# Kernel optimization log

Measured on AMD Instinct MI355X. Metric: run time of the kernel, lower is better.

The kernel has to match this reference:

```python
import jax, jax.numpy as jnp
import numpy as np

N = 8192
NFEAT = 512
NHID = 512
NCLASS = 8
EPS = 1e-9
ADJ_P = 0.01  # edge density


def setup_inputs() -> dict:
    key = jax.random.key(0)
    ks = jax.random.split(key, 16)
    adj = (jax.random.uniform(ks[0], (N, N)) < ADJ_P).astype(jnp.float32)
    x = jax.random.normal(ks[1], (N, NFEAT), dtype=jnp.float32)
    s_in = 1.0 / np.sqrt(NFEAT)
    s_h = 1.0 / np.sqrt(NHID)
    return {
        "adj": adj,
        "x": x,
        "gcn1_W": jax.random.normal(ks[2], (NFEAT, NHID), jnp.float32) * s_in,
        "gcn1_b": jnp.zeros((NHID,), jnp.float32),
        "Qw": jax.random.normal(ks[3], (NHID, NHID), jnp.float32) * s_h,
        "Qb": jnp.zeros((NHID,), jnp.float32),
        "Kw": jax.random.normal(ks[4], (NHID, NHID), jnp.float32) * s_h,
        "Kb": jnp.zeros((NHID,), jnp.float32),
        "Vw": jax.random.normal(ks[5], (NHID, NHID), jnp.float32) * s_h,
        "Vb": jnp.zeros((NHID,), jnp.float32),
        "ln_g": jnp.ones((NHID,), jnp.float32),
        "ln_b": jnp.zeros((NHID,), jnp.float32),
        "gcn2_W": jax.random.normal(ks[6], (NHID, NCLASS), jnp.float32) * s_h,
        "gcn2_b": jnp.zeros((NCLASS,), jnp.float32),
    }


def _gcn_norm(a):
    # symmetric degree normalization D^{-1/2} A D^{-1/2}, degrees = row sums
    d_inv_sqrt = jax.lax.rsqrt(a.sum(axis=1) + EPS)  # [N]
    return d_inv_sqrt[:, None] * a * d_inv_sqrt[None, :]


def _layer_norm(x, g, b):
    mu = x.mean(axis=-1, keepdims=True)
    var = x.var(axis=-1, keepdims=True)
    return (x - mu) * jax.lax.rsqrt(var + 1e-5) * g + b


def reference(adj, x, gcn1_W, gcn1_b, Qw, Qb, Kw, Kb, Vw, Vb, ln_g, ln_b, gcn2_W, gcn2_b):
    # GraphConvolution: adj @ (x W) + b, then ReLU
    h = jax.nn.relu(adj @ (x @ gcn1_W) + gcn1_b)  # [N, NHID]
    Qh = h @ Qw + Qb
    Kh = h @ Kw + Kb
    Vh = h @ Vw + Vb
    # adjacency-masked dense scores (multiplicative mask, as in original)
    A_tilde = adj * (Qh @ Kh.T)  # [N, N]
    attention = jax.nn.softmax(A_tilde, axis=1)
    X_tilde = _gcn_norm(attention) @ Vh  # [N, NHID]
    X_tilde = _layer_norm(X_tilde, ln_g, ln_b)
    z = adj @ (X_tilde @ gcn2_W) + gcn2_b  # [N, NCLASS]
    return jax.nn.softmax(z, axis=1)
```

## Files before the change

kernel.cpp:

```cpp
#include <hip/hip_runtime.h>
#include <math.h>

#define N_NODES 8192
#define NFEAT 512
#define NHID 512
#define NCLASS 8
#define RCAP 192
#define KB_SPLIT 1536
#define KA_SPLIT 1024

__device__ inline ushort f2bf(float f) {
  uint32_t u = __float_as_uint(f);
  uint32_t r = u + 0x7fffu + ((u >> 16) & 1u);
  return (ushort)(r >> 16);
}
__device__ inline float bf2f(ushort h) { return __uint_as_float(((uint32_t)h) << 16); }

__global__ __launch_bounds__(256) void build_ell(const float* __restrict__ adj,
                                                 int* __restrict__ colidx,
                                                 int* __restrict__ deg) {
  int row = blockIdx.x;
  __shared__ int cnt;
  __shared__ int cols[RCAP];
  if (threadIdx.x == 0) cnt = 0;
  __syncthreads();
  const float4* arow = (const float4*)(adj + (size_t)row * N_NODES);
  for (int i = threadIdx.x; i < N_NODES / 4; i += 256) {
    float4 v = arow[i];
    int base = i * 4;
    if (v.x > 0.5f) { int p = atomicAdd(&cnt, 1); if (p < RCAP) cols[p] = base; }
    if (v.y > 0.5f) { int p = atomicAdd(&cnt, 1); if (p < RCAP) cols[p] = base + 1; }
    if (v.z > 0.5f) { int p = atomicAdd(&cnt, 1); if (p < RCAP) cols[p] = base + 2; }
    if (v.w > 0.5f) { int p = atomicAdd(&cnt, 1); if (p < RCAP) cols[p] = base + 3; }
  }
  __syncthreads();
  int d = cnt < RCAP ? cnt : RCAP;
  if (threadIdx.x == 0) deg[row] = d;
  for (int i = threadIdx.x; i < d; i += 256) colidx[(size_t)row * RCAP + i] = cols[i];
}

__global__ void transpose512(const float* __restrict__ in, float* __restrict__ out) {
  __shared__ float tile[32][33];
  int x = blockIdx.x * 32 + threadIdx.x;
  int y0 = blockIdx.y * 32;
  for (int i = threadIdx.y; i < 32; i += 8)
    tile[i][threadIdx.x] = in[(size_t)(y0 + i) * 512 + x];
  __syncthreads();
  int xo = blockIdx.y * 32 + threadIdx.x;
  int yo0 = blockIdx.x * 32;
  for (int i = threadIdx.y; i < 32; i += 8)
    out[(size_t)(yo0 + i) * 512 + xo] = tile[threadIdx.x][i];
}

__global__ __launch_bounds__(256) void sgemm64x128(const float* __restrict__ A,
                                                   const float* __restrict__ B,
                                                   float* __restrict__ C,
                                                   int M, int Nn, int K, int ldc) {
  __shared__ float As[16][68];
  __shared__ float Bs[16][132];
  const int tid = threadIdx.x;
  const int bm = blockIdx.y * 64, bn = blockIdx.x * 128;
  const int tx = tid & 15, ty = tid >> 4;
  const int arow = tid >> 2, acol = (tid & 3) << 2;
  const int brow = tid >> 4, bcol = (tid & 15) << 2;
  float acc[4][8];
#pragma unroll
  for (int i = 0; i < 4; ++i)
#pragma unroll
    for (int j = 0; j < 8; ++j) acc[i][j] = 0.f;
  const float* Ap = A + (size_t)(bm + arow) * K + acol;
  const float* Bp = B + (size_t)brow * Nn + bn + bcol;
  float4 av = *(const float4*)(Ap);
  float4 bv0 = *(const float4*)(Bp);
  float4 bv1 = *(const float4*)(Bp + 64);
  for (int k0 = 0; k0 < K; k0 += 16) {
    if (k0) __syncthreads();
    As[acol + 0][arow] = av.x;
    As[acol + 1][arow] = av.y;
    As[acol + 2][arow] = av.z;
    As[acol + 3][arow] = av.w;
    *(float4*)&Bs[brow][bcol] = bv0;
    *(float4*)&Bs[brow][bcol + 64] = bv1;
    __syncthreads();
    int kn = (k0 + 16 < K) ? k0 + 16 : 0;
    av = *(const float4*)(Ap + kn);
    bv0 = *(const float4*)(Bp + (size_t)kn * Nn);
    bv1 = *(const float4*)(Bp + (size_t)kn * Nn + 64);
#pragma unroll
    for (int kk = 0; kk < 16; ++kk) {
      float4 a = *(const float4*)&As[kk][ty << 2];
      float4 b0 = *(const float4*)&Bs[kk][tx << 2];
      float4 b1 = *(const float4*)&Bs[kk][(tx << 2) + 64];
// ... 96 lines not shown
    for (int j = 0; j < 4; ++j) acc[i][j] = (frag_cd){0.f, 0.f, 0.f, 0.f};

  const int srow = (w << 3) + (lane >> 3);
  const int scolb = (lane & 7) << 4;
  const uint8_t* gA = (const uint8_t*)A + (size_t)(m0 + srow) * (KA_SPLIT * 2) + scolb;
  const uint8_t* gB = (const uint8_t*)Bt + (size_t)(n0 + srow) * (KB_SPLIT * 2) + scolb;

  for (int c = 0; c < 24; ++c) {
    const size_t kaB = (size_t)((c < 8 ? c : c - 8) * 128);
    const size_t kbB = (size_t)(c * 128);
#pragma unroll
    for (int r = 0; r < 4; ++r) {
      __builtin_amdgcn_global_load_lds(
          (const __attribute__((address_space(1))) uint32_t*)(gA + (size_t)(r * 32) * (KA_SPLIT * 2) + kaB),
          (__attribute__((address_space(3))) uint32_t*)((uint8_t*)Atile + r * 4096 + w * 1024), 16, 0, 0);
      __builtin_amdgcn_global_load_lds(
          (const __attribute__((address_space(1))) uint32_t*)(gB + (size_t)(r * 32) * (KB_SPLIT * 2) + kbB),
          (__attribute__((address_space(3))) uint32_t*)((uint8_t*)Btile + r * 4096 + w * 1024), 16, 0, 0);
    }
    __syncthreads();
#pragma unroll
    for (int kk = 0; kk < 2; ++kk) {
      frag_ab af[4], bf[4];
#pragma unroll
      for (int i = 0; i < 4; ++i) {
        af[i] = *(const frag_ab*)((const uint8_t*)Atile + (wm + i * 16 + c16) * 128 + kk * 64 + q * 16);
        bf[i] = *(const frag_ab*)((const uint8_t*)Btile + (wn + i * 16 + c16) * 128 + kk * 64 + q * 16);
      }
#pragma unroll
      for (int i = 0; i < 4; ++i)
#pragma unroll
        for (int j = 0; j < 4; ++j)
          acc[i][j] = __builtin_amdgcn_mfma_f32_16x16x32_bf16(af[i], bf[j], acc[i][j], 0, 0, 0);
    }
    __syncthreads();
  }
#pragma unroll
  for (int j = 0; j < 4; ++j) {
    int col = n0 + wn + j * 16 + c16;
    float bv = bias ? bias[col] : 0.f;
    float csum = 0.f;
#pragma unroll
    for (int i = 0; i < 4; ++i) {
      int row = m0 + wm + i * 16 + q * 4;
#pragma unroll
      for (int r = 0; r < 4; ++r) {
        float v = acc[i][j][r] + bv;
        C[(size_t)(row + r) * ldc + col] = v;
        csum += v;
      }
    }
    if (Tsum && col >= 512) {
      csum += __shfl_xor(csum, 16, 64);
      csum += __shfl_xor(csum, 32, 64);
      if (q == 0) atomicAdd(&Tsum[col - 512], csum);
    }
  }
}

__global__ __launch_bounds__(64) void bias_prep(const float* __restrict__ Qw, const float* __restrict__ Kw,
                                                const float* __restrict__ Qb, const float* __restrict__ Kb,
                                                float* __restrict__ u, float* __restrict__ w,
                                                float* __restrict__ cbuf) {
  int k = blockIdx.x;
  int lane = threadIdx.x;
  if (k == NHID) {
    float s = 0.f;
    for (int j = lane; j < NHID; j += 64) s = fmaf(Qb[j], Kb[j], s);
#pragma unroll
    for (int o = 32; o > 0; o >>= 1) s += __shfl_down(s, o, 64);
    if (lane == 0) cbuf[0] = s;
    return;
  }
  float su = 0.f, sw = 0.f;
  for (int j = lane; j < NHID; j += 64) {
    su = fmaf(Qw[(size_t)k * NHID + j], Kb[j], su);
    sw = fmaf(Kw[(size_t)k * NHID + j], Qb[j], sw);
  }
#pragma unroll
  for (int o = 32; o > 0; o >>= 1) { su += __shfl_down(su, o, 64); sw += __shfl_down(sw, o, 64); }
  if (lane == 0) { u[k] = su; w[k] = sw; }
}

__global__ __launch_bounds__(128) void spmm_fused(const float* __restrict__ xW,
                                                  const int* __restrict__ colidx,
                                                  const int* __restrict__ deg,
                                                  const float* __restrict__ b1,
                                                  const float* __restrict__ u, const float* __restrict__ w,
                                                  float* __restrict__ h, ushort* __restrict__ Hs,
                                                  float* __restrict__ a_vec, float* __restrict__ b_vec) {
  __shared__ int bls[512];
  __shared__ int bcnt[8];
  __shared__ float ra[2], rb[2];
  int row = blockIdx.x, t = threadIdx.x;
  int d = deg[row];
  if (t < 8) bcnt[t] = 0;
  __syncthreads();
  for (int i = t; i < d; i += 128) {
    int c = colidx[(size_t)row * RCAP + i];
    int s = c >> 10;
    int p = atomicAdd(&bcnt[s], 1);
    bls[(s << 6) | p] = c;
  }
  __syncthreads();
  float4 acc = make_float4(0.f, 0.f, 0.f, 0.f);
  int xcd = blockIdx.x & 7;
  for (int k = 0; k < 8; ++k) {
    int s = (xcd + k) & 7;
    int n = bcnt[s];
    const int* bp = &bls[s << 6];
    int e = 0;
    for (; e + 4 <= n; e += 4) {
      float4 v0 = ((const float4*)(xW + (size_t)bp[e + 0] * NHID))[t];
      float4 v1 = ((const float4*)(xW + (size_t)bp[e + 1] * NHID))[t];
      float4 v2 = ((const float4*)(xW + (size_t)bp[e + 2] * NHID))[t];
      float4 v3 = ((const float4*)(xW + (size_t)bp[e + 3] * NHID))[t];
      acc.x += (v0.x + v1.x) + (v2.x + v3.x);
      acc.y += (v0.y + v1.y) + (v2.y + v3.y);
      acc.z += (v0.z + v1.z) + (v2.z + v3.z);
      acc.w += (v0.w + v1.w) + (v2.w + v3.w);
    }
    for (; e < n; ++e) {
      float4 v = ((const float4*)(xW + (size_t)bp[e] * NHID))[t];
      acc.x += v.x; acc.y += v.y; acc.z += v.z; acc.w += v.w;
    }
  }
  float4 bv = ((const float4*)b1)[t];
  float4 o = make_float4(fmaxf(acc.x + bv.x, 0.f), fmaxf(acc.y + bv.y, 0.f),
                         fmaxf(acc.z + bv.z, 0.f), fmaxf(acc.w + bv.w, 0.f));
  ((float4*)(h + (size_t)row * NHID))[t] = o;
  ushort4 hi, lo;
  hi.x = f2bf(o.x); hi.y = f2bf(o.y); hi.z = f2bf(o.z); hi.w = f2bf(o.w);
  lo.x = f2bf(o.x - bf2f(hi.x)); lo.y = f2bf(o.y - bf2f(hi.y));
  lo.z = f2bf(o.z - bf2f(hi.z)); lo.w = f2bf(o.w - bf2f(hi.w));
  ushort* hr = Hs + (size_t)row * KA_SPLIT;
  ((ushort4*)hr)[t] = hi;
  ((ushort4*)(hr + 512))[t] = lo;
  float4 uv = ((const float4*)u)[t], wv4 = ((const float4*)w)[t];
  float sa = fmaf(o.x, uv.x, fmaf(o.y, uv.y, fmaf(o.z, uv.z, o.w * uv.w)));
  float sb = fmaf(o.x, wv4.x, fmaf(o.y, wv4.y, fmaf(o.z, wv4.z, o.w * wv4.w)));
  int wv = t >> 6, lane = t & 63;
#pragma unroll
  for (int off = 32; off > 0; off >>= 1) { sa += __shfl_down(sa, off, 64); sb += __shfl_down(sb, off, 64); }
  if (lane == 0) { ra[wv] = sa; rb[wv] = sb; }
  __syncthreads();
  if (t == 0) { a_vec[row] = ra[0] + ra[1]; b_vec[row] = rb[0] + rb[1]; }
}

__global__ void zero_vec(float* __restrict__ T) { T[threadIdx.x] = 0.f; }

__global__ __launch_bounds__(256) void score_softmax_agg_ln(
    const float* __restrict__ G, int ldg, const float* __restrict__ h,
    const int* __restrict__ colidx, const int* __restrict__ deg,
    const float* __restrict__ a_vec, const float* __restrict__ b_vec,
    const float* __restrict__ cbuf, const float* __restrict__ Vh, int ldv,
    const float* __restrict__ T, const float* __restrict__ lng,
    const float* __restrict__ lnb, float* __restrict__ Xt) {
  __shared__ float gs[4][NHID];
  __shared__ int bls[4][512];
  __shared__ int bcnt[4][8];
  __shared__ int scols[4][RCAP];
  __shared__ float sv[4][RCAP];
  int t = threadIdx.x, wv = t >> 6, lane = t & 63;
  int row = blockIdx.x * 4 + wv;
  int d = deg[row];
  if (lane < 8) bcnt[wv][lane] = 0;
  const float4* gr = (const float4*)(G + (size_t)row * ldg);
  ((float4*)gs[wv])[lane] = gr[lane];
  ((float4*)gs[wv])[64 + lane] = gr[64 + lane];
  __syncthreads();
  for (int i = lane; i < d; i += 64) {
    int c = colidx[(size_t)row * RCAP + i];
    scols[wv][i] = c;
    int s = c >> 10;
    int p = atomicAdd(&bcnt[wv][s], 1);
    bls[wv][(s << 6) | p] = (c << 8) | i;
  }
  __syncthreads();
  float ai = a_vec[row] + cbuf[0];
  int xcd = blockIdx.x & 7;
  int q = lane >> 4, u = lane & 15;
  const float4* gq = (const float4*)gs[wv] + u;
  for (int k = 0; k < 8; ++k) {
    int s = (xcd + k) & 7;
    int n = bcnt[wv][s];
    for (int e0 = 0; e0 < n; e0 += 4) {
      int idx = e0 + q;
      bool act = idx < n;
      int pack = bls[wv][(s << 6) | (act ? idx : 0)];
      int col = pack >> 8;
      const float4* hr = (const float4*)(h + (size_t)col * NHID) + u;
      float s_a = 0.f, s_b = 0.f;
#pragma unroll
      for (int it = 0; it < 8; it += 2) {
        float4 h0 = hr[it * 16], g0 = gq[it * 16];
        float4 h1 = hr[(it + 1) * 16], g1 = gq[(it + 1) * 16];
        s_a = fmaf(h0.x, g0.x, s_a); s_a = fmaf(h0.y, g0.y, s_a);
        s_a = fmaf(h0.z, g0.z, s_a); s_a = fmaf(h0.w, g0.w, s_a);
        s_b = fmaf(h1.x, g1.x, s_b); s_b = fmaf(h1.y, g1.y, s_b);
        s_b = fmaf(h1.z, g1.z, s_b); s_b = fmaf(h1.w, g1.w, s_b);
      }
      float sc = s_a + s_b;
      sc += __shfl_down(sc, 8, 16);
      sc += __shfl_down(sc, 4, 16);
      sc += __shfl_down(sc, 2, 16);
      sc += __shfl_down(sc, 1, 16);
      if (u == 0 && act) sv[wv][pack & 255] = sc + ai + b_vec[col];
    }
  }
  __syncthreads();
  float m = 0.f;
  for (int i = lane; i < d; i += 64) m = fmaxf(m, sv[wv][i]);
#pragma unroll
  for (int o = 32; o > 0; o >>= 1) m = fmaxf(m, __shfl_xor(m, o, 64));
  float ssum = 0.f;
  for (int i = lane; i < d; i += 64) {
    float ex = expf(sv[wv][i] - m);
    sv[wv][i] = ex;
    ssum += ex;
  }
#pragma unroll
  for (int o = 32; o > 0; o >>= 1) ssum += __shfl_xor(ssum, o, 64);
  float em = expf(-m);
  float inv = 1.f / (ssum + (float)(N_NODES - d) * em);
  float ci = em * inv;
  __syncthreads();
  float4 a0 = make_float4(0.f, 0.f, 0.f, 0.f), a1 = a0;
  for (int e = 0; e < d; ++e) {
    float we = sv[wv][e] * inv;
    if (we > 1e-12f) {
      const float4* vr = (const float4*)(Vh + (size_t)scols[wv][e] * ldv);
      float4 v0 = vr[lane * 2], v1 = vr[lane * 2 + 1];
      a0.x = fmaf(we, v0.x, a0.x); a0.y = fmaf(we, v0.y, a0.y);
      a0.z = fmaf(we, v0.z, a0.z); a0.w = fmaf(we, v0.w, a0.w);
      a1.x = fmaf(we, v1.x, a1.x); a1.y = fmaf(we, v1.y, a1.y);
      a1.z = fmaf(we, v1.z, a1.z); a1.w = fmaf(we, v1.w, a1.w);
    }
  }
  float4 t0 = ((const float4*)T)[lane * 2], t1 = ((const float4*)T)[lane * 2 + 1];
  a0.x = fmaf(ci, t0.x, a0.x); a0.y = fmaf(ci, t0.y, a0.y);
  a0.z = fmaf(ci, t0.z, a0.z); a0.w = fmaf(ci, t0.w, a0.w);
  a1.x = fmaf(ci, t1.x, a1.x); a1.y = fmaf(ci, t1.y, a1.y);
  a1.z = fmaf(ci, t1.z, a1.z); a1.w = fmaf(ci, t1.w, a1.w);
  float s1 = ((a0.x + a0.y) + (a0.z + a0.w)) + ((a1.x + a1.y) + (a1.z + a1.w));
  float s2 = ((a0.x * a0.x + a0.y * a0.y) + (a0.z * a0.z + a0.w * a0.w)) +
             ((a1.x * a1.x + a1.y * a1.y) + (a1.z * a1.z + a1.w * a1.w));
#pragma unroll
  for (int o = 32; o > 0; o >>= 1) { s1 += __shfl_xor(s1, o, 64); s2 += __shfl_xor(s2, o, 64); }
  float mu = s1 * (1.f / NHID);
  float var = s2 * (1.f / NHID) - mu * mu;
  float rstd = rsqrtf(var + 1e-5f);
  float4 g0 = ((const float4*)lng)[lane * 2], g1 = ((const float4*)lng)[lane * 2 + 1];
  float4 b0 = ((const float4*)lnb)[lane * 2], b1 = ((const float4*)lnb)[lane * 2 + 1];
  float4 o0, o1;
  o0.x = (a0.x - mu) * rstd * g0.x + b0.x;
  o0.y = (a0.y - mu) * rstd * g0.y + b0.y;
  o0.z = (a0.z - mu) * rstd * g0.z + b0.z;
  o0.w = (a0.w - mu) * rstd * g0.w + b0.w;
  o1.x = (a1.x - mu) * rstd * g1.x + b1.x;
  o1.y = (a1.y - mu) * rstd * g1.y + b1.y;
  o1.z = (a1.z - mu) * rstd * g1.z + b1.z;
  o1.w = (a1.w - mu) * rstd * g1.w + b1.w;
  float4* xr = (float4*)(Xt + (size_t)row * NHID);
  xr[lane * 2] = o0;
  xr[lane * 2 + 1] = o1;
}

__global__ __launch_bounds__(256) void xt_w2(const float* __restrict__ Xt, const float* __restrict__ W2,
                                             float* __restrict__ Y) {
  __shared__ float w2s[NHID * NCLASS];
  int t = threadIdx.x;
  for (int i = t; i < NHID * NCLASS; i += 256) w2s[i] = W2[i];
  __syncthreads();
  int wv = t >> 6, lane = t & 63;
  int row = blockIdx.x * 4 + wv;
  const float4* xr = (const float4*)(Xt + (size_t)row * NHID);
  float4 x0 = xr[lane * 2], x1 = xr[lane * 2 + 1];
  float xv[8] = {x0.x, x0.y, x0.z, x0.w, x1.x, x1.y, x1.z, x1.w};
  float acc[NCLASS];
#pragma unroll
  for (int c = 0; c < NCLASS; ++c) acc[c] = 0.f;
#pragma unroll
  for (int kk = 0; kk < 8; ++kk) {
    int k = lane * 8 + kk;
#pragma unroll
    for (int c = 0; c < NCLASS; ++c) acc[c] = fmaf(xv[kk], w2s[k * NCLASS + c], acc[c]);
  }
#pragma unroll
  for (int c = 0; c < NCLASS; ++c)
#pragma unroll
    for (int o = 32; o > 0; o >>= 1) acc[c] += __shfl_down(acc[c], o, 64);
  if (lane == 0) {
    *(float4*)(Y + (size_t)row * NCLASS) = make_float4(acc[0], acc[1], acc[2], acc[3]);
    *(float4*)(Y + (size_t)row * NCLASS + 4) = make_float4(acc[4], acc[5], acc[6], acc[7]);
  }
}

__global__ __launch_bounds__(256) void final_spmm_softmax(const float* __restrict__ Y,
                                                          const int* __restrict__ colidx,
                                                          const int* __restrict__ deg,
                                                          const float* __restrict__ b2,
                                                          float* __restrict__ out) {
  int t = threadIdx.x;
  int wv = t >> 6, lane = t & 63;
  int row = blockIdx.x * 4 + wv;
  int d = deg[row];
  const int* cols = colidx + (size_t)row * RCAP;
  float acc[8];
#pragma unroll
  for (int c = 0; c < 8; ++c) acc[c] = 0.f;
  for (int e = lane; e < d; e += 64) {
    int col = cols[e];
    const float4* yr = (const float4*)(Y + (size_t)col * 8);
    float4 y0 = yr[0], y1 = yr[1];
    acc[0] += y0.x; acc[1] += y0.y; acc[2] += y0.z; acc[3] += y0.w;
    acc[4] += y1.x; acc[5] += y1.y; acc[6] += y1.z; acc[7] += y1.w;
  }
#pragma unroll
  for (int c = 0; c < 8; ++c)
#pragma unroll
    for (int o = 32; o > 0; o >>= 1) acc[c] += __shfl_down(acc[c], o, 64);
  if (lane == 0) {
    float z[8];
    float m = -1e30f;
#pragma unroll
    for (int c = 0; c < 8; ++c) { z[c] = acc[c] + b2[c]; m = fmaxf(m, z[c]); }
    float s = 0.f;
#pragma unroll
    for (int c = 0; c < 8; ++c) { z[c] = expf(z[c] - m); s += z[c]; }
    float inv = 1.f / s;
    *(float4*)(out + (size_t)row * 8) = make_float4(z[0] * inv, z[1] * inv, z[2] * inv, z[3] * inv);
    *(float4*)(out + (size_t)row * 8 + 4) = make_float4(z[4] * inv, z[5] * inv, z[6] * inv, z[7] * inv);
  }
}

extern "C" void kernel_launch(void* const* d_in, const int* in_sizes, int n_in,
                              void* d_out, int out_size, void* d_ws, size_t ws_size,
                              hipStream_t stream) {
  const float* adj = (const float*)d_in[0];
  const float* x = (const float*)d_in[1];
  const float* W1 = (const float*)d_in[2];
  const float* b1 = (const float*)d_in[3];
  const float* Qw = (const float*)d_in[4];
  const float* Qb = (const float*)d_in[5];
  const float* Kw = (const float*)d_in[6];
  const float* Kb = (const float*)d_in[7];
  const float* Vw = (const float*)d_in[8];
  const float* Vb = (const float*)d_in[9];
  const float* ln_g = (const float*)d_in[10];
  const float* ln_b = (const float*)d_in[11];
  const float* W2 = (const float*)d_in[12];
  const float* b2 = (const float*)d_in[13];
  float* out = (float*)d_out;

  char* ws = (char*)d_ws;
  size_t off = 0;
  auto alloc = [&](size_t bytes) -> void* {
    void* p = ws + off;
    off = (off + bytes + 255) & ~(size_t)255;
    return p;
  };
  int* colidx = (int*)alloc((size_t)N_NODES * RCAP * 4);
  int* deg = (int*)alloc((size_t)N_NODES * 4);
  float* bufA = (float*)alloc((size_t)N_NODES * NHID * 4);
  float* bufB = (float*)alloc((size_t)N_NODES * NHID * 4);
  float* GVh = (float*)alloc((size_t)N_NODES * 1024 * 4);
  ushort* Xs = (ushort*)alloc((size_t)N_NODES * KA_SPLIT * 2);
  ushort* Hs = (ushort*)alloc((size_t)N_NODES * KA_SPLIT * 2);
  ushort* W1ts = (ushort*)alloc((size_t)512 * KB_SPLIT * 2);
  ushort* Bcts = (ushort*)alloc((size_t)1024 * KB_SPLIT * 2);
  float* KwT = (float*)alloc((size_t)512 * 512 * 4);
  float* Mmat = (float*)alloc((size_t)512 * 512 * 4);
  float* bcat = (float*)alloc((size_t)1024 * 4);
  float* a_vec = (float*)alloc((size_t)N_NODES * 4);
  float* b_vec = (float*)alloc((size_t)N_NODES * 4);
  float* u_vec = (float*)alloc((size_t)NHID * 4);
  float* w_vec = (float*)alloc((size_t)NHID * 4);
  float* cbuf = (float*)alloc(256);
  float* T = (float*)alloc((size_t)NHID * 4);
  float* Y = (float*)alloc((size_t)N_NODES * NCLASS * 4);
  (void)in_sizes; (void)n_in; (void)out_size; (void)ws_size;

  build_ell<<<N_NODES, 256, 0, stream>>>(adj, colidx, deg);
  transpose512<<<dim3(16, 16), dim3(32, 8), 0, stream>>>(Kw, KwT);
  bias_prep<<<NHID + 1, 64, 0, stream>>>(Qw, Kw, Qb, Kb, u_vec, w_vec, cbuf);
  sgemm64x128<<<dim3(4, 8), 256, 0, stream>>>(Qw, KwT, Mmat, 512, 512, 512, 512);
  split_a2<<<(N_NODES * 128) / 256, 256, 0, stream>>>(x, Xs);
  split_bt<<<(512 * 384) / 256, 256, 0, stream>>>(W1, W1ts, 512);
  mfma_gemm_bt<<<dim3(4, 64), 256, 0, stream>>>(Xs, W1ts, nullptr, bufA, 512, nullptr);
  spmm_fused<<<N_NODES, 128, 0, stream>>>(bufA, colidx, deg, b1, u_vec, w_vec, bufB, Hs, a_vec, b_vec);
  split_bt_cat<<<(1024 * 384) / 256, 256, 0, stream>>>(Mmat, Vw, Bcts);
  build_bcat<<<4, 256, 0, stream>>>(Vb, bcat);
  zero_vec<<<1, 512, 0, stream>>>(T);
  mfma_gemm_bt<<<dim3(8, 64), 256, 0, stream>>>(Hs, Bcts, bcat, GVh, 1024, T);
  score_softmax_agg_ln<<<N_NODES / 4, 256, 0, stream>>>(GVh, 1024, bufB, colidx, deg, a_vec, b_vec,
                                                        cbuf, GVh + 512, 1024, T, ln_g, ln_b, bufA);
  xt_w2<<<N_NODES / 4, 256, 0, stream>>>(bufA, W2, Y);
  final_spmm_softmax<<<N_NODES / 4, 256, 0, stream>>>(Y, colidx, deg, b2, out);
}
```

Baseline: 803.3 us.

## Use cooperative grid syncs to phase sparse gathers by column slice for L2 locality

The two sparse gather kernels now process several rows per block, and they become cooperative launches that call grid.sync between the eight column-slice phases. The aim is to keep every block reading the same 1024-row slice of the gathered matrix at once, so that slice stays resident in cache. The score kernel also keeps the query row in registers instead of shared memory, and adds the row bias after the gather. Bucket capacities are now clamped to 64 and 48 entries, which silently drops neighbours if a slice overflows, and the seven grid barriers add synchronisation cost.

```diff
diff --git a/kernel.cpp b/kernel.cpp
--- a/kernel.cpp
+++ b/kernel.cpp
@@ -1,5 +1,8 @@
 #include <hip/hip_runtime.h>
+#include <hip/hip_cooperative_groups.h>
 #include <math.h>
+
+namespace cg = cooperative_groups;
 
 #define N_NODES 8192
 #define NFEAT 512
@@ -270,188 +273,223 @@
   if (lane == 0) { u[k] = su; w[k] = sw; }
 }
 
-__global__ __launch_bounds__(128) void spmm_fused(const float* __restrict__ xW,
-                                                  const int* __restrict__ colidx,
-                                                  const int* __restrict__ deg,
-                                                  const float* __restrict__ b1,
-                                                  const float* __restrict__ u, const float* __restrict__ w,
-                                                  float* __restrict__ h, ushort* __restrict__ Hs,
-                                                  float* __restrict__ a_vec, float* __restrict__ b_vec) {
-  __shared__ int bls[512];
-  __shared__ int bcnt[8];
-  __shared__ float ra[2], rb[2];
-  int row = blockIdx.x, t = threadIdx.x;
-  int d = deg[row];
-  if (t < 8) bcnt[t] = 0;
-  __syncthreads();
-  for (int i = t; i < d; i += 128) {
-    int c = colidx[(size_t)row * RCAP + i];
-    int s = c >> 10;
-    int p = atomicAdd(&bcnt[s], 1);
-    bls[(s << 6) | p] = c;
-  }
-  __syncthreads();
-  float4 acc = make_float4(0.f, 0.f, 0.f, 0.f);
+__global__ __launch_bounds__(128) void spmm_coop(const float* __restrict__ xW,
+                                                 const int* __restrict__ colidx,
+                                                 const int* __restrict__ deg,
+                                                 const float* __restrict__ b1,
+                                                 const float* __restrict__ u, const float* __restrict__ w,
+                                                 float* __restrict__ h, ushort* __restrict__ Hs,
+                                                 float* __restrict__ a_vec, float* __restrict__ b_vec,
+                                                 int use_sync) {
+  cg::grid_group grid = cg::this_grid();
+  __shared__ int bls[4][8][64];
+  __shared__ int bcnt[4][8];
+  __shared__ float ra[4][2], rb[4][2];
+  int t = threadIdx.x;
+  int row0 = blockIdx.x * 4;
+  if (t < 32) bcnt[t >> 3][t & 7] = 0;
+  __syncthreads();
+  for (int r = 0; r < 4; ++r) {
+    int d = deg[row0 + r];
+    for (int i = t; i < d; i += 128) {
+      int c = colidx[(size_t)(row0 + r) * RCAP + i];
+      int s = c >> 10;
+      int p = atomicAdd(&bcnt[r][s], 1);
+      if (p < 64) bls[r][s][p] = c;
+    }
+  }
+  __syncthreads();
+  float4 acc[4];
+#pragma unroll
+  for (int r = 0; r < 4; ++r) acc[r] = make_float4(0.f, 0.f, 0.f, 0.f);
   int xcd = blockIdx.x & 7;
   for (int k = 0; k < 8; ++k) {
     int s = (xcd + k) & 7;
-    int n = bcnt[s];
-    const int* bp = &bls[s << 6];
-    int e = 0;
-    for (; e + 4 <= n; e += 4) {
-      float4 v0 = ((const float4*)(xW + (size_t)bp[e + 0] * NHID))[t];
-      float4 v1 = ((const float4*)(xW + (size_t)bp[e + 1] * NHID))[t];
-      float4 v2 = ((const float4*)(xW + (size_t)bp[e + 2] * NHID))[t];
-      float4 v3 = ((const float4*)(xW + (size_t)bp[e + 3] * NHID))[t];
-      acc.x += (v0.x + v1.x) + (v2.x + v3.x);
-      acc.y += (v0.y + v1.y) + (v2.y + v3.y);
-      acc.z += (v0.z + v1.z) + (v2.z + v3.z);
-      acc.w += (v0.w + v1.w) + (v2.w + v3.w);
-    }
-    for (; e < n; ++e) {
-      float4 v = ((const float4*)(xW + (size_t)bp[e] * NHID))[t];
-      acc.x += v.x; acc.y += v.y; acc.z += v.z; acc.w += v.w;
-    }
-  }
+#pragma unroll
+    for (int r = 0; r < 4; ++r) {
+      int n = bcnt[r][s]; n = n < 64 ? n : 64;
+      const int* bp = bls[r][s];
+      int e = 0;
+      for (; e + 4 <= n; e += 4) {
+        float4 v0 = ((const float4*)(xW + (size_t)bp[e + 0] * NHID))[t];
+        float4 v1 = ((const float4*)(xW + (size_t)bp[e + 1] * NHID))[t];
+        float4 v2 = ((const float4*)(xW + (size_t)bp[e + 2] * NHID))[t];
+        float4 v3 = ((const float4*)(xW + (size_t)bp[e + 3] * NHID))[t];
+        acc[r].x += (v0.x + v1.x) + (v2.x + v3.x);
+        acc[r].y += (v0.y + v1.y) + (v2.y + v3.y);
+        acc[r].z += (v0.z + v1.z) + (v2.z + v3.z);
+        acc[r].w += (v0.w + v1.w) + (v2.w + v3.w);
+      }
+      for (; e < n; ++e) {
+        float4 v = ((const float4*)(xW + (size_t)bp[e] * NHID))[t];
+        acc[r].x += v.x; acc[r].y += v.y; acc[r].z += v.z; acc[r].w += v.w;
+      }
+    }
+    if (use_sync && k < 7) grid.sync();
+  }
+  int wv = t >> 6, lane = t & 63;
   float4 bv = ((const float4*)b1)[t];
-  float4 o = make_float4(fmaxf(acc.x + bv.x, 0.f), fmaxf(acc.y + bv.y, 0.f),
-                         fmaxf(acc.z + bv.z, 0.f), fmaxf(acc.w + bv.w, 0.f));
-  ((float4*)(h + (size_t)row * NHID))[t] = o;
-  ushort4 hi, lo;
-  hi.x = f2bf(o.x); hi.y = f2bf(o.y); hi.z = f2bf(o.z); hi.w = f2bf(o.w);
-  lo.x = f2bf(o.x - bf2f(hi.x)); lo.y = f2bf(o.y - bf2f(hi.y));
-  lo.z = f2bf(o.z - bf2f(hi.z)); lo.w = f2bf(o.w - bf2f(hi.w));
-  ushort* hr = Hs + (size_t)row * KA_SPLIT;
-  ((ushort4*)hr)[t] = hi;
-  ((ushort4*)(hr + 512))[t] = lo;
-  float4 uv = ((const float4*)u)[t], wv4 = ((const float4*)w)[t];
-  float sa = fmaf(o.x, uv.x, fmaf(o.y, uv.y, fmaf(o.z, uv.z, o.w * uv.w)));
-  float sb = fmaf(o.x, wv4.x, fmaf(o.y, wv4.y, fmaf(o.z, wv4.z, o.w * wv4.w)));
-  int wv = t >> 6, lane = t & 63;
-#pragma unroll
-  for (int off = 32; off > 0; off >>= 1) { sa += __shfl_down(sa, off, 64); sb += __shfl_down(sb, off, 64); }
-  if (lane == 0) { ra[wv] = sa; rb[wv] = sb; }
-  __syncthreads();
-  if (t == 0) { a_vec[row] = ra[0] + ra[1]; b_vec[row] = rb[0] + rb[1]; }
+  float4 uv = ((const float4*)u)[t];
+  float4 wv4 = ((const float4*)w)[t];
+#pragma unroll
+  for (int r = 0; r < 4; ++r) {
+    int row = row0 + r;
+    float4 o = make_float4(fmaxf(acc[r].x + bv.x, 0.f), fmaxf(acc[r].y + bv.y, 0.f),
+                           fmaxf(acc[r].z + bv.z, 0.f), fmaxf(acc[r].w + bv.w, 0.f));
+    ((float4*)(h + (size_t)row * NHID))[t] = o;
+    ushort4 hi, lo;
+    hi.x = f2bf(o.x); hi.y = f2bf(o.y); hi.z = f2bf(o.z); hi.w = f2bf(o.w);
+    lo.x = f2bf(o.x - bf2f(hi.x)); lo.y = f2bf(o.y - bf2f(hi.y));
+    lo.z = f2bf(o.z - bf2f(hi.z)); lo.w = f2bf(o.w - bf2f(hi.w));
+    ushort* hr = Hs + (size_t)row * KA_SPLIT;
+    ((ushort4*)hr)[t] = hi;
+    ((ushort4*)(hr + 512))[t] = lo;
+    float sa = fmaf(o.x, uv.x, fmaf(o.y, uv.y, fmaf(o.z, uv.z, o.w * uv.w)));
+    float sb = fmaf(o.x, wv4.x, fmaf(o.y, wv4.y, fmaf(o.z, wv4.z, o.w * wv4.w)));
+#pragma unroll
+    for (int off = 32; off > 0; off >>= 1) {
+      sa += __shfl_down(sa, off, 64);
+      sb += __shfl_down(sb, off, 64);
+    }
+    if (lane == 0) { ra[r][wv] = sa; rb[r][wv] = sb; }
+  }
+  __syncthreads();
+  if (t < 4) {
+    a_vec[row0 + t] = ra[t][0] + ra[t][1];
+    b_vec[row0 + t] = rb[t][0] + rb[t][1];
+  }
 }
 
 __global__ void zero_vec(float* __restrict__ T) { T[threadIdx.x] = 0.f; }
 
-__global__ __launch_bounds__(256) void score_softmax_agg_ln(
+__global__ __launch_bounds__(256) void score_coop(
     const float* __restrict__ G, int ldg, const float* __restrict__ h,
     const int* __restrict__ colidx, const int* __restrict__ deg,
     const float* __restrict__ a_vec, const float* __restrict__ b_vec,
     const float* __restrict__ cbuf, const float* __restrict__ Vh, int ldv,
     const float* __restrict__ T, const float* __restrict__ lng,
-    const float* __restrict__ lnb, float* __restrict__ Xt) {
-  __shared__ float gs[4][NHID];
-  __shared__ int bls[4][512];
-  __shared__ int bcnt[4][8];
-  __shared__ int scols[4][RCAP];
-  __shared__ float sv[4][RCAP];
+    const float* __restrict__ lnb, float* __restrict__ Xt, int use_sync) {
+  cg::grid_group grid = cg::this_grid();
+  __shared__ int bls[8][8][48];
+  __shared__ int bcnt[8][8];
+  __shared__ int scols[8][RCAP];
+  __shared__ float sv[8][RCAP];
   int t = threadIdx.x, wv = t >> 6, lane = t & 63;
-  int row = blockIdx.x * 4 + wv;
-  int d = deg[row];
-  if (lane < 8) bcnt[wv][lane] = 0;
-  const float4* gr = (const float4*)(G + (size_t)row * ldg);
-  ((float4*)gs[wv])[lane] = gr[lane];
-  ((float4*)gs[wv])[64 + lane] = gr[64 + lane];
-  __syncthreads();
-  for (int i = lane; i < d; i += 64) {
-    int c = colidx[(size_t)row * RCAP + i];
-    scols[wv][i] = c;
-    int s = c >> 10;
-    int p = atomicAdd(&bcnt[wv][s], 1);
-    bls[wv][(s << 6) | p] = (c << 8) | i;
-  }
-  __syncthreads();
-  float ai = a_vec[row] + cbuf[0];
+  int rowA = blockIdx.x * 8 + wv * 2;
+  int q = lane >> 4, u = lane & 15;
+  if (lane < 16) bcnt[wv * 2 + (lane >> 3)][lane & 7] = 0;
+  __syncthreads();
+  float4 gfrag[2][8];
+#pragma unroll
+  for (int r = 0; r < 2; ++r) {
+    const float4* Gr = (const float4*)(G + (size_t)(rowA + r) * ldg);
+#pragma unroll
+    for (int it = 0; it < 8; ++it) gfrag[r][it] = Gr[it * 16 + u];
+  }
+  for (int r = 0; r < 2; ++r) {
+    int row = rowA + r, rr = wv * 2 + r;
+    int d = deg[row];
+    for (int i = lane; i < d; i += 64) {
+      int c = colidx[(size_t)row * RCAP + i];
+      scols[rr][i] = c;
+      int s = c >> 10;
+      int p = atomicAdd(&bcnt[rr][s], 1);
+      if (p < 48) bls[rr][s][p] = (c << 8) | i;
+    }
+  }
+  __syncthreads();
   int xcd = blockIdx.x & 7;
-  int q = lane >> 4, u = lane & 15;
-  const float4* gq = (const float4*)gs[wv] + u;
   for (int k = 0; k < 8; ++k) {
     int s = (xcd + k) & 7;
-    int n = bcnt[wv][s];
-    for (int e0 = 0; e0 < n; e0 += 4) {
-      int idx = e0 + q;
-      bool act = idx < n;
-      int pack = bls[wv][(s << 6) | (act ? idx : 0)];
-      int col = pack >> 8;
-      const float4* hr = (const float4*)(h + (size_t)col * NHID) + u;
-      float s_a = 0.f, s_b = 0.f;
-#pragma unroll
-      for (int it = 0; it < 8; it += 2) {
-        float4 h0 = hr[it * 16], g0 = gq[it * 16];
-        float4 h1 = hr[(it + 1) * 16], g1 = gq[(it + 1) * 16];
-        s_a = fmaf(h0.x, g0.x, s_a); s_a = fmaf(h0.y, g0.y, s_a);
-        s_a = fmaf(h0.z, g0.z, s_a); s_a = fmaf(h0.w, g0.w, s_a);
-        s_b = fmaf(h1.x, g1.x, s_b); s_b = fmaf(h1.y, g1.y, s_b);
-        s_b = fmaf(h1.z, g1.z, s_b); s_b = fmaf(h1.w, g1.w, s_b);
+#pragma unroll
+    for (int r = 0; r < 2; ++r) {
+      int rr = wv * 2 + r;
+      int n = bcnt[rr][s]; n = n < 48 ? n : 48;
+      for (int e0 = 0; e0 < n; e0 += 4) {
+        int idx = e0 + q;
+        bool act = idx < n;
+        int pack = bls[rr][s][act ? idx : 0];
+        int col = pack >> 8;
+        const float4* hr = (const float4*)(h + (size_t)col * NHID) + u;
+        float s_a = 0.f, s_b = 0.f;
+#pragma unroll
+        for (int it = 0; it < 8; it += 2) {
+          float4 h0 = hr[it * 16], h1 = hr[(it + 1) * 16];
+          float4 g0 = gfrag[r][it], g1 = gfrag[r][it + 1];
+          s_a = fmaf(h0.x, g0.x, s_a); s_a = fmaf(h0.y, g0.y, s_a);
+          s_a = fmaf(h0.z, g0.z, s_a); s_a = fmaf(h0.w, g0.w, s_a);
+          s_b = fmaf(h1.x, g1.x, s_b); s_b = fmaf(h1.y, g1.y, s_b);
+          s_b = fmaf(h1.z, g1.z, s_b); s_b = fmaf(h1.w, g1.w, s_b);
+        }
+        float sc = s_a + s_b;
+        sc += __shfl_down(sc, 8, 16);
+        sc += __shfl_down(sc, 4, 16);
+        sc += __shfl_down(sc, 2, 16);
+        sc += __shfl_down(sc, 1, 16);
+        if (u == 0 && act) sv[rr][pack & 255] = sc + b_vec[col];
       }
-      float sc = s_a + s_b;
-      sc += __shfl_down(sc, 8, 16);
-      sc += __shfl_down(sc, 4, 16);
-      sc += __shfl_down(sc, 2, 16);
-      sc += __shfl_down(sc, 1, 16);
-      if (u == 0 && act) sv[wv][pack & 255] = sc + ai + b_vec[col];
-    }
-  }
-  __syncthreads();
-  float m = 0.f;
-  for (int i = lane; i < d; i += 64) m = fmaxf(m, sv[wv][i]);
-#pragma unroll
-  for (int o = 32; o > 0; o >>= 1) m = fmaxf(m, __shfl_xor(m, o, 64));
-  float ssum = 0.f;
-  for (int i = lane; i < d; i += 64) {
-    float ex = expf(sv[wv][i] - m);
-    sv[wv][i] = ex;
-    ssum += ex;
-  }
-#pragma unroll
-  for (int o = 32; o > 0; o >>= 1) ssum += __shfl_xor(ssum, o, 64);
-  float em = expf(-m);
-  float inv = 1.f / (ssum + (float)(N_NODES - d) * em);
-  float ci = em * inv;
-  __syncthreads();
-  float4 a0 = make_float4(0.f, 0.f, 0.f, 0.f), a1 = a0;
-  for (int e = 0; e < d; ++e) {
-    float we = sv[wv][e] * inv;
-    if (we > 1e-12f) {
-      const float4* vr = (const float4*)(Vh + (size_t)scols[wv][e] * ldv);
-      float4 v0 = vr[lane * 2], v1 = vr[lane * 2 + 1];
-      a0.x = fmaf(we, v0.x, a0.x); a0.y = fmaf(we, v0.y, a0.y);
-      a0.z = fmaf(we, v0.z, a0.z); a0.w = fmaf(we, v0.w, a0.w);
-      a1.x = fmaf(we, v1.x, a1.x); a1.y = fmaf(we, v1.y, a1.y);
-      a1.z = fmaf(we, v1.z, a1.z); a1.w = fmaf(we, v1.w, a1.w);
-    }
-  }
-  float4 t0 = ((const float4*)T)[lane * 2], t1 = ((const float4*)T)[lane * 2 + 1];
-  a0.x = fmaf(ci, t0.x, a0.x); a0.y = fmaf(ci, t0.y, a0.y);
-  a0.z = fmaf(ci, t0.z, a0.z); a0.w = fmaf(ci, t0.w, a0.w);
-  a1.x = fmaf(ci, t1.x, a1.x); a1.y = fmaf(ci, t1.y, a1.y);
-  a1.z = fmaf(ci, t1.z, a1.z); a1.w = fmaf(ci, t1.w, a1.w);
-  float s1 = ((a0.x + a0.y) + (a0.z + a0.w)) + ((a1.x + a1.y) + (a1.z + a1.w));
-  float s2 = ((a0.x * a0.x + a0.y * a0.y) + (a0.z * a0.z + a0.w * a0.w)) +
-             ((a1.x * a1.x + a1.y * a1.y) + (a1.z * a1.z + a1.w * a1.w));
-#pragma unroll
-  for (int o = 32; o > 0; o >>= 1) { s1 += __shfl_xor(s1, o, 64); s2 += __shfl_xor(s2, o, 64); }
-  float mu = s1 * (1.f / NHID);
-  float var = s2 * (1.f / NHID) - mu * mu;
-  float rstd = rsqrtf(var + 1e-5f);
-  float4 g0 = ((const float4*)lng)[lane * 2], g1 = ((const float4*)lng)[lane * 2 + 1];
-  float4 b0 = ((const float4*)lnb)[lane * 2], b1 = ((const float4*)lnb)[lane * 2 + 1];
-  float4 o0, o1;
-  o0.x = (a0.x - mu) * rstd * g0.x + b0.x;
-  o0.y = (a0.y - mu) * rstd * g0.y + b0.y;
-  o0.z = (a0.z - mu) * rstd * g0.z + b0.z;
-  o0.w = (a0.w - mu) * rstd * g0.w + b0.w;
-  o1.x = (a1.x - mu) * rstd * g1.x + b1.x;
-  o1.y = (a1.y - mu) * rstd * g1.y + b1.y;
-  o1.z = (a1.z - mu) * rstd * g1.z + b1.z;
-  o1.w = (a1.w - mu) * rstd * g1.w + b1.w;
-  float4* xr = (float4*)(Xt + (size_t)row * NHID);
-  xr[lane * 2] = o0;
-  xr[lane * 2 + 1] = o1;
+    }
+    if (use_sync && k < 7) grid.sync();
+  }
+  for (int r = 0; r < 2; ++r) {
+    int row = rowA + r, rr = wv * 2 + r;
+    int d = deg[row];
+    float aic = a_vec[row] + cbuf[0];
+    float m = 0.f;
+    for (int i = lane; i < d; i += 64) { float x = sv[rr][i] + aic; sv[rr][i] = x; m = fmaxf(m, x); }
+#pragma unroll
+    for (int o = 32; o > 0; o >>= 1) m = fmaxf(m, __shfl_xor(m, o, 64));
+    float ssum = 0.f;
+    for (int i = lane; i < d; i += 64) {
+      float ex = expf(sv[rr][i] - m);
+      sv[rr][i] = ex;
+      ssum += ex;
+    }
+#pragma unroll
+    for (int o = 32; o > 0; o >>= 1) ssum += __shfl_xor(ssum, o, 64);
+    float em = expf(-m);
+    float inv = 1.f / (ssum + (float)(N_NODES - d) * em);
+    float ci = em * inv;
+    float4 a0 = make_float4(0.f, 0.f, 0.f, 0.f), a1 = a0;
+    for (int e = 0; e < d; ++e) {
+      float we = sv[rr][e] * inv;
+      if (we > 1e-12f) {
+        const float4* vr = (const float4*)(Vh + (size_t)scols[rr][e] * ldv);
+        float4 v0 = vr[lane * 2], v1 = vr[lane * 2 + 1];
+        a0.x = fmaf(we, v0.x, a0.x); a0.y = fmaf(we, v0.y, a0.y);
+        a0.z = fmaf(we, v0.z, a0.z); a0.w = fmaf(we, v0.w, a0.w);
+        a1.x = fmaf(we, v1.x, a1.x); a1.y = fmaf(we, v1.y, a1.y);
+        a1.z = fmaf(we, v1.z, a1.z); a1.w = fmaf(we, v1.w, a1.w);
+      }
+    }
+    float4 t0 = ((const float4*)T)[lane * 2], t1 = ((const float4*)T)[lane * 2 + 1];
+    a0.x = fmaf(ci, t0.x, a0.x); a0.y = fmaf(ci, t0.y, a0.y);
+    a0.z = fmaf(ci, t0.z, a0.z); a0.w = fmaf(ci, t0.w, a0.w);
+    a1.x = fmaf(ci, t1.x, a1.x); a1.y = fmaf(ci, t1.y, a1.y);
+    a1.z = fmaf(ci, t1.z, a1.z); a1.w = fmaf(ci, t1.w, a1.w);
+    float s1 = ((a0.x + a0.y) + (a0.z + a0.w)) + ((a1.x + a1.y) + (a1.z + a1.w));
+    float s2 = ((a0.x * a0.x + a0.y * a0.y) + (a0.z * a0.z + a0.w * a0.w)) +
+               ((a1.x * a1.x + a1.y * a1.y) + (a1.z * a1.z + a1.w * a1.w));
+#pragma unroll
+    for (int o = 32; o > 0; o >>= 1) { s1 += __shfl_xor(s1, o, 64); s2 += __shfl_xor(s2, o, 64); }
+    float mu = s1 * (1.f / NHID);
+    float var = s2 * (1.f / NHID) - mu * mu;
+    float rstd = rsqrtf(var + 1e-5f);
+    float4 g0 = ((const float4*)lng)[lane * 2], g1 = ((const float4*)lng)[lane * 2 + 1];
+    float4 b0 = ((const float4*)lnb)[lane * 2], b1 = ((const float4*)lnb)[lane * 2 + 1];
+    float4 o0, o1;
+    o0.x = (a0.x - mu) * rstd * g0.x + b0.x;
+    o0.y = (a0.y - mu) * rstd * g0.y + b0.y;
+    o0.z = (a0.z - mu) * rstd * g0.z + b0.z;
+    o0.w = (a0.w - mu) * rstd * g0.w + b0.w;
+    o1.x = (a1.x - mu) * rstd * g1.x + b1.x;
+    o1.y = (a1.y - mu) * rstd * g1.y + b1.y;
+    o1.z = (a1.z - mu) * rstd * g1.z + b1.z;
+    o1.w = (a1.w - mu) * rstd * g1.w + b1.w;
+    float4* xr = (float4*)(Xt + (size_t)row * NHID);
+    xr[lane * 2] = o0;
+    xr[lane * 2 + 1] = o1;
+  }
 }
 
 __global__ __launch_bounds__(256) void xt_w2(const float* __restrict__ Xt, const float* __restrict__ W2,
@@ -576,13 +614,45 @@
   split_a2<<<(N_NODES * 128) / 256, 256, 0, stream>>>(x, Xs);
   split_bt<<<(512 * 384) / 256, 256, 0, stream>>>(W1, W1ts, 512);
   mfma_gemm_bt<<<dim3(4, 64), 256, 0, stream>>>(Xs, W1ts, nullptr, bufA, 512, nullptr);
-  spmm_fused<<<N_NODES, 128, 0, stream>>>(bufA, colidx, deg, b1, u_vec, w_vec, bufB, Hs, a_vec, b_vec);
+
+  int nb_a = 0, nb_b = 0;
+  (void)hipOccupancyMaxActiveBlocksPerMultiprocessor(&nb_a, (const void*)spmm_coop, 128, 0);
+  (void)hipOccupancyMaxActiveBlocksPerMultiprocessor(&nb_b, (const void*)score_coop, 256, 0);
+  int sync_a = (nb_a * 256 >= 2048) ? 1 : 0;
+  int sync_b = (nb_b * 256 >= 1024) ? 1 : 0;
+
+  {
+    const float* p_xW = bufA; const int* p_ci = colidx; const int* p_dg = deg;
+    float* p_h = bufB;
+    if (sync_a) {
+      void* args[] = {(void*)&p_xW, (void*)&p_ci, (void*)&p_dg, (void*)&b1, (void*)&u_vec,
+                      (void*)&w_vec, (void*)&p_h, (void*)&Hs, (void*)&a_vec, (void*)&b_vec,
+                      (void*)&sync_a};
+      (void)hipLaunchCooperativeKernel((void*)spmm_coop, dim3(N_NODES / 4), dim3(128), args, 0, stream);
+    } else {
+      spmm_coop<<<N_NODES / 4, 128, 0, stream>>>(p_xW, p_ci, p_dg, b1, u_vec, w_vec, p_h, Hs,
+                                                 a_vec, b_vec, 0);
+    }
+  }
   split_bt_cat<<<(1024 * 384) / 256, 256, 0, stream>>>(Mmat, Vw, Bcts);
   build_bcat<<<4, 256, 0, stream>>>(Vb, bcat);
   zero_vec<<<1, 512, 0, stream>>>(T);
   mfma_gemm_bt<<<dim3(8, 64), 256, 0, stream>>>(Hs, Bcts, bcat, GVh, 1024, T);
-  score_softmax_agg_ln<<<N_NODES / 4, 256, 0, stream>>>(GVh, 1024, bufB, colidx, deg, a_vec, b_vec,
-                                                        cbuf, GVh + 512, 1024, T, ln_g, ln_b, bufA);
+  {
+    const float* p_G = GVh; const float* p_h = bufB; const float* p_Vh = GVh + 512;
+    const int* p_ci = colidx; const int* p_dg = deg;
+    float* p_Xt = bufA;
+    int ldg = 1024, ldv = 1024;
+    if (sync_b) {
+      void* args[] = {(void*)&p_G, (void*)&ldg, (void*)&p_h, (void*)&p_ci, (void*)&p_dg,
+                      (void*)&a_vec, (void*)&b_vec, (void*)&cbuf, (void*)&p_Vh, (void*)&ldv,
+                      (void*)&T, (void*)&ln_g, (void*)&ln_b, (void*)&p_Xt, (void*)&sync_b};
+      (void)hipLaunchCooperativeKernel((void*)score_coop, dim3(N_NODES / 8), dim3(256), args, 0, stream);
+    } else {
+      score_coop<<<N_NODES / 8, 256, 0, stream>>>(p_G, ldg, p_h, p_ci, p_dg, a_vec, b_vec, cbuf,
+                                                  p_Vh, ldv, T, ln_g, ln_b, p_Xt, 0);
+    }
+  }
   xt_w2<<<N_NODES / 4, 256, 0, stream>>>(bufA, W2, Y);
   final_spmm_softmax<<<N_NODES / 4, 256, 0, stream>>>(Y, colidx, deg, b2, out);
 }
```

Result: slower. 2.419 ms (+201.1%).

## Two-pass score filtering with bf16 pre-scores and simplify spmm gather

Applied to the files above, without the earlier changes.

The score kernel first computes approximate edge scores from the bf16 high half of h, keeps only candidates within a fixed margin of the row maximum, and recomputes exact fp32 scores only for those before softmax and V aggregation. Non-candidate edges are dropped from the softmax sum and aggregation on the assumption that their weight is negligible. This is meant to cut the fp32 h gathers and the V gathers, at the cost of an extra pass and a heuristic that relies on large score spreads, with a full fallback when the candidate list overflows. The first SpMM also drops the XCD-bucketed neighbor ordering in favor of a plain shared-memory column list and 8-way unrolled gathers.

```diff
diff --git a/kernel.cpp b/kernel.cpp
--- a/kernel.cpp
+++ b/kernel.cpp
@@ -8,6 +8,8 @@
 #define RCAP 192
 #define KB_SPLIT 1536
 #define KA_SPLIT 1024
+#define CANDCAP 64
+#define FILTER_MARGIN 96.0f
 
 __device__ inline ushort f2bf(float f) {
   uint32_t u = __float_as_uint(f);
@@ -277,41 +279,31 @@
                                                   const float* __restrict__ u, const float* __restrict__ w,
                                                   float* __restrict__ h, ushort* __restrict__ Hs,
                                                   float* __restrict__ a_vec, float* __restrict__ b_vec) {
-  __shared__ int bls[512];
-  __shared__ int bcnt[8];
+  __shared__ int scols[RCAP];
   __shared__ float ra[2], rb[2];
   int row = blockIdx.x, t = threadIdx.x;
   int d = deg[row];
-  if (t < 8) bcnt[t] = 0;
-  __syncthreads();
-  for (int i = t; i < d; i += 128) {
-    int c = colidx[(size_t)row * RCAP + i];
-    int s = c >> 10;
-    int p = atomicAdd(&bcnt[s], 1);
-    bls[(s << 6) | p] = c;
-  }
+  for (int i = t; i < d; i += 128) scols[i] = colidx[(size_t)row * RCAP + i];
   __syncthreads();
   float4 acc = make_float4(0.f, 0.f, 0.f, 0.f);
-  int xcd = blockIdx.x & 7;
-  for (int k = 0; k < 8; ++k) {
-    int s = (xcd + k) & 7;
-    int n = bcnt[s];
-    const int* bp = &bls[s << 6];
-    int e = 0;
-    for (; e + 4 <= n; e += 4) {
-      float4 v0 = ((const float4*)(xW + (size_t)bp[e + 0] * NHID))[t];
-      float4 v1 = ((const float4*)(xW + (size_t)bp[e + 1] * NHID))[t];
-      float4 v2 = ((const float4*)(xW + (size_t)bp[e + 2] * NHID))[t];
-      float4 v3 = ((const float4*)(xW + (size_t)bp[e + 3] * NHID))[t];
-      acc.x += (v0.x + v1.x) + (v2.x + v3.x);
-      acc.y += (v0.y + v1.y) + (v2.y + v3.y);
-      acc.z += (v0.z + v1.z) + (v2.z + v3.z);
-      acc.w += (v0.w + v1.w) + (v2.w + v3.w);
-    }
-    for (; e < n; ++e) {
-      float4 v = ((const float4*)(xW + (size_t)bp[e] * NHID))[t];
-      acc.x += v.x; acc.y += v.y; acc.z += v.z; acc.w += v.w;
-    }
+  int e = 0;
+  for (; e + 8 <= d; e += 8) {
+    float4 v0 = ((const float4*)(xW + (size_t)scols[e + 0] * NHID))[t];
+    float4 v1 = ((const float4*)(xW + (size_t)scols[e + 1] * NHID))[t];
+    float4 v2 = ((const float4*)(xW + (size_t)scols[e + 2] * NHID))[t];
+    float4 v3 = ((const float4*)(xW + (size_t)scols[e + 3] * NHID))[t];
+    float4 v4 = ((const float4*)(xW + (size_t)scols[e + 4] * NHID))[t];
+    float4 v5 = ((const float4*)(xW + (size_t)scols[e + 5] * NHID))[t];
+    float4 v6 = ((const float4*)(xW + (size_t)scols[e + 6] * NHID))[t];
+    float4 v7 = ((const float4*)(xW + (size_t)scols[e + 7] * NHID))[t];
+    acc.x += ((v0.x + v1.x) + (v2.x + v3.x)) + ((v4.x + v5.x) + (v6.x + v7.x));
+    acc.y += ((v0.y + v1.y) + (v2.y + v3.y)) + ((v4.y + v5.y) + (v6.y + v7.y));
+    acc.z += ((v0.z + v1.z) + (v2.z + v3.z)) + ((v4.z + v5.z) + (v6.z + v7.z));
+    acc.w += ((v0.w + v1.w) + (v2.w + v3.w)) + ((v4.w + v5.w) + (v6.w + v7.w));
+  }
+  for (; e < d; ++e) {
+    float4 v = ((const float4*)(xW + (size_t)scols[e] * NHID))[t];
+    acc.x += v.x; acc.y += v.y; acc.z += v.z; acc.w += v.w;
   }
   float4 bv = ((const float4*)b1)[t];
   float4 o = make_float4(fmaxf(acc.x + bv.x, 0.f), fmaxf(acc.y + bv.y, 0.f),
@@ -337,74 +329,114 @@
 
 __global__ void zero_vec(float* __restrict__ T) { T[threadIdx.x] = 0.f; }
 
-__global__ __launch_bounds__(256) void score_softmax_agg_ln(
+__global__ __launch_bounds__(256) void score2_agg_ln(
     const float* __restrict__ G, int ldg, const float* __restrict__ h,
-    const int* __restrict__ colidx, const int* __restrict__ deg,
+    const ushort* __restrict__ Hs, const int* __restrict__ colidx, const int* __restrict__ deg,
     const float* __restrict__ a_vec, const float* __restrict__ b_vec,
     const float* __restrict__ cbuf, const float* __restrict__ Vh, int ldv,
     const float* __restrict__ T, const float* __restrict__ lng,
     const float* __restrict__ lnb, float* __restrict__ Xt) {
-  __shared__ float gs[4][NHID];
-  __shared__ int bls[4][512];
-  __shared__ int bcnt[4][8];
   __shared__ int scols[4][RCAP];
+  __shared__ float sbv[4][RCAP];
   __shared__ float sv[4][RCAP];
+  __shared__ int cand[4][CANDCAP];
+  __shared__ int ccnt[4];
   int t = threadIdx.x, wv = t >> 6, lane = t & 63;
   int row = blockIdx.x * 4 + wv;
   int d = deg[row];
-  if (lane < 8) bcnt[wv][lane] = 0;
-  const float4* gr = (const float4*)(G + (size_t)row * ldg);
-  ((float4*)gs[wv])[lane] = gr[lane];
-  ((float4*)gs[wv])[64 + lane] = gr[64 + lane];
-  __syncthreads();
+  int q = lane >> 4, u = lane & 15;
+  if (lane == 0) ccnt[wv] = 0;
+  float4 ga4[4][2];
+  const float4* Gr4 = (const float4*)(G + (size_t)row * ldg);
+#pragma unroll
+  for (int it2 = 0; it2 < 4; ++it2) {
+    ga4[it2][0] = Gr4[it2 * 32 + 2 * u];
+    ga4[it2][1] = Gr4[it2 * 32 + 2 * u + 1];
+  }
   for (int i = lane; i < d; i += 64) {
     int c = colidx[(size_t)row * RCAP + i];
     scols[wv][i] = c;
-    int s = c >> 10;
-    int p = atomicAdd(&bcnt[wv][s], 1);
-    bls[wv][(s << 6) | p] = (c << 8) | i;
-  }
-  __syncthreads();
+    sbv[wv][i] = b_vec[c];
+  }
+  __syncthreads();
+  for (int e0 = 0; e0 < d; e0 += 4) {
+    int e = e0 + q;
+    bool act = e < d;
+    int col = scols[wv][act ? e : 0];
+    const uint4* hr = (const uint4*)(Hs + (size_t)col * KA_SPLIT);
+    float s_a = 0.f, s_b = 0.f;
+#pragma unroll
+    for (int it2 = 0; it2 < 4; ++it2) {
+      uint4 p = hr[it2 * 16 + u];
+      float4 g0 = ga4[it2][0], g1 = ga4[it2][1];
+      s_a = fmaf(__uint_as_float(p.x << 16), g0.x, s_a);
+      s_a = fmaf(__uint_as_float(p.x & 0xffff0000u), g0.y, s_a);
+      s_a = fmaf(__uint_as_float(p.y << 16), g0.z, s_a);
+      s_a = fmaf(__uint_as_float(p.y & 0xffff0000u), g0.w, s_a);
+      s_b = fmaf(__uint_as_float(p.z << 16), g1.x, s_b);
+      s_b = fmaf(__uint_as_float(p.z & 0xffff0000u), g1.y, s_b);
+      s_b = fmaf(__uint_as_float(p.w << 16), g1.z, s_b);
+      s_b = fmaf(__uint_as_float(p.w & 0xffff0000u), g1.w, s_b);
+    }
+    float s = s_a + s_b;
+    s += __shfl_down(s, 8, 16);
+    s += __shfl_down(s, 4, 16);
+    s += __shfl_down(s, 2, 16);
+    s += __shfl_down(s, 1, 16);
+    if (u == 0 && act) sv[wv][e] = s + sbv[wv][e];
+  }
+  __syncthreads();
+  float fm = -1e30f;
+  for (int i = lane; i < d; i += 64) fm = fmaxf(fm, sv[wv][i]);
+#pragma unroll
+  for (int o = 32; o > 0; o >>= 1) fm = fmaxf(fm, __shfl_xor(fm, o, 64));
+  for (int i = lane; i < d; i += 64) {
+    if (sv[wv][i] >= fm - FILTER_MARGIN) {
+      int p = atomicAdd(&ccnt[wv], 1);
+      if (p < CANDCAP) cand[wv][p] = i;
+    }
+  }
+  __syncthreads();
+  int nc = ccnt[wv];
+  bool ovf = nc > CANDCAP;
+  if (ovf) nc = d;
   float ai = a_vec[row] + cbuf[0];
-  int xcd = blockIdx.x & 7;
-  int q = lane >> 4, u = lane & 15;
-  const float4* gq = (const float4*)gs[wv] + u;
-  for (int k = 0; k < 8; ++k) {
-    int s = (xcd + k) & 7;
-    int n = bcnt[wv][s];
-    for (int e0 = 0; e0 < n; e0 += 4) {
-      int idx = e0 + q;
-      bool act = idx < n;
-      int pack = bls[wv][(s << 6) | (act ? idx : 0)];
-      int col = pack >> 8;
-      const float4* hr = (const float4*)(h + (size_t)col * NHID) + u;
-      float s_a = 0.f, s_b = 0.f;
-#pragma unroll
-      for (int it = 0; it < 8; it += 2) {
-        float4 h0 = hr[it * 16], g0 = gq[it * 16];
-        float4 h1 = hr[(it + 1) * 16], g1 = gq[(it + 1) * 16];
-        s_a = fmaf(h0.x, g0.x, s_a); s_a = fmaf(h0.y, g0.y, s_a);
-        s_a = fmaf(h0.z, g0.z, s_a); s_a = fmaf(h0.w, g0.w, s_a);
-        s_b = fmaf(h1.x, g1.x, s_b); s_b = fmaf(h1.y, g1.y, s_b);
-        s_b = fmaf(h1.z, g1.z, s_b); s_b = fmaf(h1.w, g1.w, s_b);
-      }
-      float sc = s_a + s_b;
-      sc += __shfl_down(sc, 8, 16);
-      sc += __shfl_down(sc, 4, 16);
-      sc += __shfl_down(sc, 2, 16);
-      sc += __shfl_down(sc, 1, 16);
-      if (u == 0 && act) sv[wv][pack & 255] = sc + ai + b_vec[col];
-    }
+  for (int c0 = 0; c0 < nc; c0 += 4) {
+    int idx = c0 + q;
+    bool act = idx < nc;
+    int e = act ? (ovf ? idx : cand[wv][idx]) : 0;
+    int col = scols[wv][e];
+    const float4* hr = (const float4*)(h + (size_t)col * NHID);
+    float s_a = 0.f, s_b = 0.f;
+#pragma unroll
+    for (int it2 = 0; it2 < 4; ++it2) {
+      float4 h0 = hr[it2 * 32 + 2 * u], h1 = hr[it2 * 32 + 2 * u + 1];
+      float4 g0 = ga4[it2][0], g1 = ga4[it2][1];
+      s_a = fmaf(h0.x, g0.x, s_a); s_a = fmaf(h0.y, g0.y, s_a);
+      s_a = fmaf(h0.z, g0.z, s_a); s_a = fmaf(h0.w, g0.w, s_a);
+      s_b = fmaf(h1.x, g1.x, s_b); s_b = fmaf(h1.y, g1.y, s_b);
+      s_b = fmaf(h1.z, g1.z, s_b); s_b = fmaf(h1.w, g1.w, s_b);
+    }
+    float s = s_a + s_b;
+    s += __shfl_down(s, 8, 16);
+    s += __shfl_down(s, 4, 16);
+    s += __shfl_down(s, 2, 16);
+    s += __shfl_down(s, 1, 16);
+    if (u == 0 && act) sv[wv][e] = s + ai + sbv[wv][e];
   }
   __syncthreads();
   float m = 0.f;
-  for (int i = lane; i < d; i += 64) m = fmaxf(m, sv[wv][i]);
+  for (int i = lane; i < nc; i += 64) {
+    int e = ovf ? i : cand[wv][i];
+    m = fmaxf(m, sv[wv][e]);
+  }
 #pragma unroll
   for (int o = 32; o > 0; o >>= 1) m = fmaxf(m, __shfl_xor(m, o, 64));
   float ssum = 0.f;
-  for (int i = lane; i < d; i += 64) {
-    float ex = expf(sv[wv][i] - m);
-    sv[wv][i] = ex;
+  for (int i = lane; i < nc; i += 64) {
+    int e = ovf ? i : cand[wv][i];
+    float ex = expf(sv[wv][e] - m);
+    sv[wv][e] = ex;
     ssum += ex;
   }
 #pragma unroll
@@ -414,7 +446,8 @@
   float ci = em * inv;
   __syncthreads();
   float4 a0 = make_float4(0.f, 0.f, 0.f, 0.f), a1 = a0;
-  for (int e = 0; e < d; ++e) {
+  for (int i = 0; i < nc; ++i) {
+    int e = ovf ? i : cand[wv][i];
     float we = sv[wv][e] * inv;
     if (we > 1e-12f) {
       const float4* vr = (const float4*)(Vh + (size_t)scols[wv][e] * ldv);
@@ -581,8 +614,8 @@
   build_bcat<<<4, 256, 0, stream>>>(Vb, bcat);
   zero_vec<<<1, 512, 0, stream>>>(T);
   mfma_gemm_bt<<<dim3(8, 64), 256, 0, stream>>>(Hs, Bcts, bcat, GVh, 1024, T);
-  score_softmax_agg_ln<<<N_NODES / 4, 256, 0, stream>>>(GVh, 1024, bufB, colidx, deg, a_vec, b_vec,
-                                                        cbuf, GVh + 512, 1024, T, ln_g, ln_b, bufA);
+  score2_agg_ln<<<N_NODES / 4, 256, 0, stream>>>(GVh, 1024, bufB, Hs, colidx, deg, a_vec, b_vec,
+                                                 cbuf, GVh + 512, 1024, T, ln_g, ln_b, bufA);
   xt_w2<<<N_NODES / 4, 256, 0, stream>>>(bufA, W2, Y);
   final_spmm_softmax<<<N_NODES / 4, 256, 0, stream>>>(Y, colidx, deg, b2, out);
 }
```

Measured after the change: 766.7 us. -4.6%, faster.
